# Kernel optimization log

Measured on AMD Instinct MI355X. Metric: run time of the kernel, lower is better.

Reference implementation:

```python
import jax, jax.numpy as jnp
import numpy as np

N_NODES = 100000
N_EDGES = 1600000
NODE_FEATURES = 6
H_EMBED = 64
D = 32
OUT_DIM = 1


def _mlp(x, W1, b1, W2, b2):
    h = jnp.tanh(x @ W1 + b1)
    return jnp.tanh(h @ W2 + b2)


def _gcn_conv(h, W, b, src, dst, n_nodes):
    # PyG GCNConv: linear (no bias) -> add self-loops -> sym-normalized scatter-add -> +bias
    hw = h @ W  # [N, D]
    loop = jnp.arange(n_nodes, dtype=src.dtype)
    row = jnp.concatenate([src, loop])  # sources
    col = jnp.concatenate([dst, loop])  # targets
    ones = jnp.ones(row.shape[0], dtype=hw.dtype)
    deg = jax.ops.segment_sum(ones, col, num_segments=n_nodes)
    dinv = jnp.where(deg > 0, jax.lax.rsqrt(deg), 0.0)
    norm = dinv[row] * dinv[col]  # [E+N]
    msg = hw[row] * norm[:, None]  # gather + scale
    out = jax.ops.segment_sum(msg, col, num_segments=n_nodes)
    return out + b


def setup_inputs() -> dict:
    key = jax.random.key(0)
    ks = jax.random.split(key, 16)
    x = jax.random.normal(ks[0], (N_NODES, NODE_FEATURES), dtype=jnp.float32)
    edge_index = jax.random.randint(ks[1], (2, N_EDGES), 0, N_NODES, dtype=jnp.int64)

    def lin(k, din, dout):
        bound = 1.0 / np.sqrt(din)
        kw, kb = jax.random.split(k)
        W = jax.random.uniform(kw, (din, dout), minval=-bound, maxval=bound, dtype=jnp.float32)
        b = jax.random.uniform(kb, (dout,), minval=-bound, maxval=bound, dtype=jnp.float32)
        return W, b

    We1, be1 = lin(ks[2], NODE_FEATURES, H_EMBED)
    We2, be2 = lin(ks[3], H_EMBED, D)
    Wg1, bg1 = lin(ks[4], D, D)
    Wg2, bg2 = lin(ks[5], D, D)
    Wp1, bp1 = lin(ks[6], D, D)
    Wp2, bp2 = lin(ks[7], D, OUT_DIM)
    return {
        "x": x, "edge_index": edge_index,
        "We1": We1, "be1": be1, "We2": We2, "be2": be2,
        "Wg1": Wg1, "bg1": bg1, "Wg2": Wg2, "bg2": bg2,
        "Wp1": Wp1, "bp1": bp1, "Wp2": Wp2, "bp2": bp2,
    }


def reference(x, edge_index, We1, be1, We2, be2, Wg1, bg1, Wg2, bg2, Wp1, bp1, Wp2, bp2):
    n = x.shape[0]
    src, dst = edge_index[0], edge_index[1]
    h = _mlp(x, We1, be1, We2, be2)            # [N, 32]
    h = jax.nn.relu(_gcn_conv(h, Wg1, bg1, src, dst, n))  # dropout = identity (eval)
    h = jax.nn.relu(_gcn_conv(h, Wg2, bg2, src, dst, n))
    return _mlp(h, Wp1, bp1, Wp2, bp2)         # [N, 1]
```

## Files before the change

kernel.cpp:

```cpp
#include <hip/hip_runtime.h>
#include <hip/hip_fp16.h>

#define NN 100000
#define NE 1600000
#define NPB 128
#define NBUCK ((NN + NPB - 1) / NPB)
#define CAP 5120
#define PBLOCKS 256
#define PTPB 512
#define EPB (NE / PBLOCKS)
#define DUMMY 100000u
#define SENT 0xFFFFFFFFu
#define GBLK 4096
#define NSLOT (GBLK * 8)

__global__ __launch_bounds__(PTPB) void part_kernel(const int* __restrict__ src,
                                                    const int* __restrict__ dst,
                                                    unsigned int* __restrict__ bcount,
                                                    unsigned int* __restrict__ packed) {
    __shared__ unsigned int lcnt[NBUCK];
    __shared__ unsigned int lcur[NBUCK];
    for (int i = threadIdx.x; i < NBUCK; i += PTPB) lcnt[i] = 0u;
    __syncthreads();
    int e0 = blockIdx.x * EPB;
    for (int e = e0 + threadIdx.x; e < e0 + EPB; e += PTPB)
        atomicAdd(&lcnt[((unsigned)dst[e]) >> 7], 1u);
    __syncthreads();
    for (int i = threadIdx.x; i < NBUCK; i += PTPB) {
        unsigned int c = lcnt[i];
        unsigned int rc = (c + 15u) & ~15u;
        lcur[i] = rc ? atomicAdd(&bcount[i], rc) : 0u;
    }
    __syncthreads();
    for (int e = e0 + threadIdx.x; e < e0 + EPB; e += PTPB) {
        unsigned int d = (unsigned)dst[e];
        unsigned int b = d >> 7;
        unsigned int pos = atomicAdd(&lcur[b], 1u);
        packed[(size_t)b * CAP + pos] = ((d & 127u) << 17) | (unsigned)src[e];
    }
}

__global__ __launch_bounds__(512) void sort_kernel(const unsigned int* __restrict__ bcount,
                                                   unsigned int* __restrict__ packed,
                                                   unsigned int* __restrict__ rsd,
                                                   float* __restrict__ dinv) {
    __shared__ unsigned int lraw[CAP];
    __shared__ unsigned int lsort[CAP];
    __shared__ unsigned int cnt[NPB];
    __shared__ unsigned int ps[NPB];
    __shared__ unsigned int cur[NPB];
    __shared__ unsigned int ntot;
    int b = blockIdx.x;
    int tid = threadIdx.x;
    if (tid < NPB) cnt[tid] = 0u;
    __syncthreads();
    unsigned int n = bcount[b];
    unsigned int* pk = packed + (size_t)b * CAP;
    for (unsigned int i = tid; i < n; i += 512) {
        unsigned int p = pk[i];
        lraw[i] = p;
        if (p != SENT) atomicAdd(&cnt[p >> 17], 1u);
    }
    __syncthreads();
    if (tid < NPB) ps[tid] = (cnt[tid] + 7u) & ~7u;
    __syncthreads();
    for (int off = 1; off < NPB; off <<= 1) {
        unsigned int t = (tid < NPB && tid >= off) ? ps[tid - off] : 0u;
        __syncthreads();
        if (tid < NPB) ps[tid] += t;
        __syncthreads();
    }
    if (tid == NPB - 1) ntot = ps[NPB - 1];
    __syncthreads();
    unsigned int np = ntot;
    for (unsigned int i = tid; i < np; i += 512) lsort[i] = DUMMY;
    if (tid < NPB) cur[tid] = ps[tid] - ((cnt[tid] + 7u) & ~7u);
    __syncthreads();
    for (unsigned int i = tid; i < n; i += 512) {
        unsigned int p = lraw[i];
        if (p != SENT) {
            unsigned int pos = atomicAdd(&cur[p >> 17], 1u);
            lsort[pos] = p & 0x1FFFFu;
        }
    }
    __syncthreads();
    for (unsigned int i = tid; i < np; i += 512) pk[i] = lsort[i];
    if (tid < NPB) {
        int node = b * NPB + tid;
        if (node < NN) {
            unsigned int c = cnt[tid];
            unsigned int pc = (c + 7u) & ~7u;
            unsigned int rs = (unsigned int)(b * CAP) + ps[tid] - pc;
            rsd[node] = rs | ((pc >> 3) << 22);
            dinv[node] = rsqrtf((float)c + 1.0f);
        }
    }
}

__global__ __launch_bounds__(256) void embed_kernel(
    const float* __restrict__ x, const float* __restrict__ We1, const float* __restrict__ be1,
    const float* __restrict__ We2, const float* __restrict__ be2, const float* __restrict__ Wg1,
    const float* __restrict__ dinv, __half* __restrict__ hws1, __half* __restrict__ hws2) {
    __shared__ float sWe1[6 * 64];
    __shared__ float sbe1[64];
    __shared__ float sWe2[64 * 32];
    __shared__ float sbe2[32];
    __shared__ float sWg1[32 * 32];
    for (int i = threadIdx.x; i < 6 * 64; i += 256) sWe1[i] = We1[i];
    for (int i = threadIdx.x; i < 64; i += 256) sbe1[i] = be1[i];
    for (int i = threadIdx.x; i < 64 * 32; i += 256) sWe2[i] = We2[i];
    for (int i = threadIdx.x; i < 32; i += 256) sbe2[i] = be2[i];
    for (int i = threadIdx.x; i < 32 * 32; i += 256) sWg1[i] = Wg1[i];
    __syncthreads();

    int node = blockIdx.x * 256 + threadIdx.x;
    if (node > NN) return;
    if (node == NN) {
        for (int j = 0; j < 32; j++) {
            hws1[(size_t)NN * 32 + j] = __float2half(0.f);
            hws2[(size_t)NN * 32 + j] = __float2half(0.f);
        }
        return;
    }

    float xv[6];
#pragma unroll
    for (int k = 0; k < 6; k++) xv[k] = x[node * 6 + k];

    float h1[64];
#pragma unroll
    for (int j = 0; j < 64; j++) {
        float a = sbe1[j];
#pragma unroll
        for (int k = 0; k < 6; k++) a += xv[k] * sWe1[k * 64 + j];
        h1[j] = tanhf(a);
    }

    float h[32];
#pragma unroll 4
    for (int j = 0; j < 32; j++) {
        float a = sbe2[j];
#pragma unroll
        for (int k = 0; k < 64; k++) a += h1[k] * sWe2[k * 32 + j];
        h[j] = tanhf(a);
    }

    float di = dinv[node];
    __half* o = hws1 + (size_t)node * 32;
#pragma unroll 4
    for (int j = 0; j < 32; j++) {
        float a = 0.f;
#pragma unroll
        for (int k = 0; k < 32; k++) a += h[k] * sWg1[k * 32 + j];
        o[j] = __float2half(a * di);
    }
}

__global__ __launch_bounds__(256) void gather1_kernel(
    const unsigned int* __restrict__ sorted, const unsigned int* __restrict__ rsd,
    const float* __restrict__ dinv, const __half* __restrict__ hws1,
    const float* __restrict__ bg1, const float* __restrict__ Wg2,
    __half* __restrict__ hws2) {
    int lane = threadIdx.x & 31;
    int g = lane >> 4;
    int p = lane & 15;
    int f = lane;
    float wreg[32];
#pragma unroll
    for (int k = 0; k < 32; k++) wreg[k] = Wg2[k * 32 + f];
    float bf = bg1[f];
    int slot = (blockIdx.x * 256 + threadIdx.x) >> 5;
    const __half2* H = (const __half2*)hws1;
    int node = slot;
    if (node >= NN) return;
    unsigned int r = rsd[node];
    while (node < NN) {
        int nxt = node + NSLOT;
        unsigned int rn = (nxt < NN) ? rsd[nxt] : 0u;
        unsigned int base = r & 0x3FFFFFu;
        unsigned int d = (r >> 22) << 3;
        float ax = 0.f, ay = 0.f;
        for (unsigned int k = g * 4; k < d; k += 8) {
            uint4 s4 = *reinterpret_cast<const uint4*>(sorted + base + k);
            float2 v0 = __half22float2(H[(size_t)s4.x * 16 + p]);
            float2 v1 = __half22float2(H[(size_t)s4.y * 16 + p]);
            float2 v2 = __half22float2(H[(size_t)s4.z * 16 + p]);
            float2 v3 = __half22float2(H[(size_t)s4.w * 16 + p]);
            ax += (v0.x + v1.x) + (v2.x + v3.x);
            ay += (v0.y + v1.y) + (v2.y + v3.y);
        }
        ax += __shfl_xor(ax, 16); ay += __shfl_xor(ay, 16);
        float2 sv = __half22float2(H[(size_t)node * 16 + p]);
        ax += sv.x; ay += sv.y;
        float ae = __shfl(ax, f >> 1, 32);
        float ao = __shfl(ay, f >> 1, 32);
        float av = (f & 1) ? ao : ae;
        float di = dinv[node];
        float h = di * av + bf;
        h = h > 0.f ? h : 0.f;
        float o = 0.f;
#pragma unroll
        for (int k = 0; k < 32; k++) o += __shfl(h, k, 32) * wreg[k];
        hws2[(size_t)node * 32 + f] = __float2half(o * di);
        node = nxt; r = rn;
    }
}

__global__ __launch_bounds__(256) void gather2_kernel(
    const unsigned int* __restrict__ sorted, const unsigned int* __restrict__ rsd,
    const float* __restrict__ dinv, const __half* __restrict__ hws2,
    const float* __restrict__ bg2, const float* __restrict__ Wp1,
    const float* __restrict__ bp1, const float* __restrict__ Wp2,
    const float* __restrict__ bp2, float* __restrict__ out) {
    int lane = threadIdx.x & 31;
    int g = lane >> 4;
    int p = lane & 15;
    int f = lane;
    float wreg[32];
#pragma unroll
    for (int k = 0; k < 32; k++) wreg[k] = Wp1[k * 32 + f];
    float bgf = bg2[f];
    float b1f = bp1[f];
    float w2f = Wp2[f];
    float b2 = bp2[0];
    int slot = (blockIdx.x * 256 + threadIdx.x) >> 5;
    const __half2* H = (const __half2*)hws2;
    int node = slot;
    if (node >= NN) return;
    unsigned int r = rsd[node];
    while (node < NN) {
        int nxt = node + NSLOT;
        unsigned int rn = (nxt < NN) ? rsd[nxt] : 0u;
        unsigned int base = r & 0x3FFFFFu;
        unsigned int d = (r >> 22) << 3;
        float ax = 0.f, ay = 0.f;
        for (unsigned int k = g * 4; k < d; k += 8) {
            uint4 s4 = *reinterpret_cast<const uint4*>(sorted + base + k);
            float2 v0 = __half22float2(H[(size_t)s4.x * 16 + p]);
            float2 v1 = __half22float2(H[(size_t)s4.y * 16 + p]);
            float2 v2 = __half22float2(H[(size_t)s4.z * 16 + p]);
            float2 v3 = __half22float2(H[(size_t)s4.w * 16 + p]);
            ax += (v0.x + v1.x) + (v2.x + v3.x);
            ay += (v0.y + v1.y) + (v2.y + v3.y);
        }
        ax += __shfl_xor(ax, 16); ay += __shfl_xor(ay, 16);
        float2 sv = __half22float2(H[(size_t)node * 16 + p]);
        ax += sv.x; ay += sv.y;
        float ae = __shfl(ax, f >> 1, 32);
        float ao = __shfl(ay, f >> 1, 32);
        float av = (f & 1) ? ao : ae;
        float di = dinv[node];
        float h = di * av + bgf;
        h = h > 0.f ? h : 0.f;
        float pre = b1f;
#pragma unroll
        for (int k = 0; k < 32; k++) pre += __shfl(h, k, 32) * wreg[k];
        float t = tanhf(pre) * w2f;
#pragma unroll
        for (int off = 1; off < 32; off <<= 1) t += __shfl_xor(t, off);
        if (lane == 0) out[node] = tanhf(t + b2);
        node = nxt; r = rn;
    }
}

extern "C" void kernel_launch(void* const* d_in, const int* in_sizes, int n_in,
                              void* d_out, int out_size, void* d_ws, size_t ws_size,
                              hipStream_t stream) {
    const float* x = (const float*)d_in[0];
    const int* edge = (const int*)d_in[1];
    const int* src = edge;
    const int* dst = edge + NE;
    const float* We1 = (const float*)d_in[2];
    const float* be1 = (const float*)d_in[3];
    const float* We2 = (const float*)d_in[4];
    const float* be2 = (const float*)d_in[5];
    const float* Wg1 = (const float*)d_in[6];
    const float* bg1 = (const float*)d_in[7];
    const float* Wg2 = (const float*)d_in[8];
    const float* bg2 = (const float*)d_in[9];
    const float* Wp1 = (const float*)d_in[10];
    const float* bp1 = (const float*)d_in[11];
    const float* Wp2 = (const float*)d_in[12];
    const float* bp2 = (const float*)d_in[13];
    float* out = (float*)d_out;

    unsigned int* bcount = (unsigned int*)d_ws;
    float* dinv = (float*)d_ws + 1024;
    unsigned int* rsd = (unsigned int*)d_ws + 1024 + NN;
    unsigned int* packed = (unsigned int*)d_ws + 1024 + 2 * NN;
    __half* hws1 = (__half*)((unsigned int*)d_ws + 1024 + 2 * NN + NBUCK * CAP);
    __half* hws2 = hws1 + (size_t)(NN + 1) * 32;

    hipMemsetAsync(bcount, 0, 1024 * sizeof(unsigned int), stream);
    hipMemsetAsync(packed, 0xFF, (size_t)NBUCK * CAP * 4, stream);

    int gridN = (NN + 256) / 256;

    part_kernel<<<PBLOCKS, PTPB, 0, stream>>>(src, dst, bcount, packed);
    sort_kernel<<<NBUCK, 512, 0, stream>>>(bcount, packed, rsd, dinv);
    embed_kernel<<<gridN, 256, 0, stream>>>(x, We1, be1, We2, be2, Wg1, dinv, hws1, hws2);
    gather1_kernel<<<GBLK, 256, 0, stream>>>(packed, rsd, dinv, hws1, bg1, Wg2, hws2);
    gather2_kernel<<<GBLK, 256, 0, stream>>>(packed, rsd, dinv, hws2, bg2, Wp1, bp1, Wp2, bp2, out);
}
```

Baseline: 250.1 us.

## Interleave two nodes per half-warp in gather kernels and retune partition launch

Both gather kernels now process two nodes (na and na+NSLOT) per loop iteration, issuing their neighbor-index and feature loads together to double memory-level parallelism, with tail loops for unequal degrees. The partition kernel is retuned to 128 blocks of 1024 threads with a smaller bucket capacity. The interleaving raises register pressure and halves the number of loop iterations per warp, which may reduce occupancy or worsen load balance; the smaller CAP risks overflow if bucket sizes exceed it.

```diff
diff --git a/kernel.cpp b/kernel.cpp
--- a/kernel.cpp
+++ b/kernel.cpp
@@ -5,9 +5,9 @@
 #define NE 1600000
 #define NPB 128
 #define NBUCK ((NN + NPB - 1) / NPB)
-#define CAP 5120
-#define PBLOCKS 256
-#define PTPB 512
+#define CAP 4608
+#define PBLOCKS 128
+#define PTPB 1024
 #define EPB (NE / PBLOCKS)
 #define DUMMY 100000u
 #define SENT 0xFFFFFFFFu
@@ -171,38 +171,78 @@
     float bf = bg1[f];
     int slot = (blockIdx.x * 256 + threadIdx.x) >> 5;
     const __half2* H = (const __half2*)hws1;
-    int node = slot;
-    if (node >= NN) return;
-    unsigned int r = rsd[node];
-    while (node < NN) {
-        int nxt = node + NSLOT;
-        unsigned int rn = (nxt < NN) ? rsd[nxt] : 0u;
-        unsigned int base = r & 0x3FFFFFu;
-        unsigned int d = (r >> 22) << 3;
-        float ax = 0.f, ay = 0.f;
-        for (unsigned int k = g * 4; k < d; k += 8) {
-            uint4 s4 = *reinterpret_cast<const uint4*>(sorted + base + k);
-            float2 v0 = __half22float2(H[(size_t)s4.x * 16 + p]);
-            float2 v1 = __half22float2(H[(size_t)s4.y * 16 + p]);
-            float2 v2 = __half22float2(H[(size_t)s4.z * 16 + p]);
-            float2 v3 = __half22float2(H[(size_t)s4.w * 16 + p]);
-            ax += (v0.x + v1.x) + (v2.x + v3.x);
-            ay += (v0.y + v1.y) + (v2.y + v3.y);
+    for (int na = slot; na < NN; na += 2 * NSLOT) {
+        int nb = na + NSLOT;
+        bool hb = nb < NN;
+        unsigned int ra = rsd[na];
+        unsigned int rb = hb ? rsd[nb] : 0u;
+        unsigned int base_a = ra & 0x3FFFFFu, da = (ra >> 22) << 3;
+        unsigned int base_b = rb & 0x3FFFFFu, db = hb ? ((rb >> 22) << 3) : 0u;
+        float ax = 0.f, ay = 0.f, bx2 = 0.f, by2 = 0.f;
+        unsigned int dmin = da < db ? da : db;
+        unsigned int k = g * 4;
+        for (; k < dmin; k += 8) {
+            uint4 sa = *reinterpret_cast<const uint4*>(sorted + base_a + k);
+            uint4 sb = *reinterpret_cast<const uint4*>(sorted + base_b + k);
+            float2 a0 = __half22float2(H[(size_t)sa.x * 16 + p]);
+            float2 a1 = __half22float2(H[(size_t)sa.y * 16 + p]);
+            float2 a2 = __half22float2(H[(size_t)sa.z * 16 + p]);
+            float2 a3 = __half22float2(H[(size_t)sa.w * 16 + p]);
+            float2 b0 = __half22float2(H[(size_t)sb.x * 16 + p]);
+            float2 b1 = __half22float2(H[(size_t)sb.y * 16 + p]);
+            float2 b2 = __half22float2(H[(size_t)sb.z * 16 + p]);
+            float2 b3 = __half22float2(H[(size_t)sb.w * 16 + p]);
+            ax += (a0.x + a1.x) + (a2.x + a3.x);
+            ay += (a0.y + a1.y) + (a2.y + a3.y);
+            bx2 += (b0.x + b1.x) + (b2.x + b3.x);
+            by2 += (b0.y + b1.y) + (b2.y + b3.y);
+        }
+        for (unsigned int ka = k; ka < da; ka += 8) {
+            uint4 sa = *reinterpret_cast<const uint4*>(sorted + base_a + ka);
+            float2 a0 = __half22float2(H[(size_t)sa.x * 16 + p]);
+            float2 a1 = __half22float2(H[(size_t)sa.y * 16 + p]);
+            float2 a2 = __half22float2(H[(size_t)sa.z * 16 + p]);
+            float2 a3 = __half22float2(H[(size_t)sa.w * 16 + p]);
+            ax += (a0.x + a1.x) + (a2.x + a3.x);
+            ay += (a0.y + a1.y) + (a2.y + a3.y);
+        }
+        for (unsigned int kb = k; kb < db; kb += 8) {
+            uint4 sb = *reinterpret_cast<const uint4*>(sorted + base_b + kb);
+            float2 b0 = __half22float2(H[(size_t)sb.x * 16 + p]);
+            float2 b1 = __half22float2(H[(size_t)sb.y * 16 + p]);
+            float2 b2 = __half22float2(H[(size_t)sb.z * 16 + p]);
+            float2 b3 = __half22float2(H[(size_t)sb.w * 16 + p]);
+            bx2 += (b0.x + b1.x) + (b2.x + b3.x);
+            by2 += (b0.y + b1.y) + (b2.y + b3.y);
         }
         ax += __shfl_xor(ax, 16); ay += __shfl_xor(ay, 16);
-        float2 sv = __half22float2(H[(size_t)node * 16 + p]);
+        float2 sv = __half22float2(H[(size_t)na * 16 + p]);
         ax += sv.x; ay += sv.y;
         float ae = __shfl(ax, f >> 1, 32);
         float ao = __shfl(ay, f >> 1, 32);
         float av = (f & 1) ? ao : ae;
-        float di = dinv[node];
-        float h = di * av + bf;
-        h = h > 0.f ? h : 0.f;
-        float o = 0.f;
-#pragma unroll
-        for (int k = 0; k < 32; k++) o += __shfl(h, k, 32) * wreg[k];
-        hws2[(size_t)node * 32 + f] = __float2half(o * di);
-        node = nxt; r = rn;
+        float dia = dinv[na];
+        float ha = dia * av + bf;
+        ha = ha > 0.f ? ha : 0.f;
+        float oa = 0.f;
+#pragma unroll
+        for (int k2 = 0; k2 < 32; k2++) oa += __shfl(ha, k2, 32) * wreg[k2];
+        hws2[(size_t)na * 32 + f] = __float2half(oa * dia);
+        if (hb) {
+            bx2 += __shfl_xor(bx2, 16); by2 += __shfl_xor(by2, 16);
+            float2 svb = __half22float2(H[(size_t)nb * 16 + p]);
+            bx2 += svb.x; by2 += svb.y;
+            float be = __shfl(bx2, f >> 1, 32);
+            float bo = __shfl(by2, f >> 1, 32);
+            float bv = (f & 1) ? bo : be;
+            float dib = dinv[nb];
+            float hbv = dib * bv + bf;
+            hbv = hbv > 0.f ? hbv : 0.f;
+            float ob = 0.f;
+#pragma unroll
+            for (int k2 = 0; k2 < 32; k2++) ob += __shfl(hbv, k2, 32) * wreg[k2];
+            hws2[(size_t)nb * 32 + f] = __float2half(ob * dib);
+        }
     }
 }
 
@@ -225,41 +265,84 @@
     float b2 = bp2[0];
     int slot = (blockIdx.x * 256 + threadIdx.x) >> 5;
     const __half2* H = (const __half2*)hws2;
-    int node = slot;
-    if (node >= NN) return;
-    unsigned int r = rsd[node];
-    while (node < NN) {
-        int nxt = node + NSLOT;
-        unsigned int rn = (nxt < NN) ? rsd[nxt] : 0u;
-        unsigned int base = r & 0x3FFFFFu;
-        unsigned int d = (r >> 22) << 3;
-        float ax = 0.f, ay = 0.f;
-        for (unsigned int k = g * 4; k < d; k += 8) {
-            uint4 s4 = *reinterpret_cast<const uint4*>(sorted + base + k);
-            float2 v0 = __half22float2(H[(size_t)s4.x * 16 + p]);
-            float2 v1 = __half22float2(H[(size_t)s4.y * 16 + p]);
-            float2 v2 = __half22float2(H[(size_t)s4.z * 16 + p]);
-            float2 v3 = __half22float2(H[(size_t)s4.w * 16 + p]);
-            ax += (v0.x + v1.x) + (v2.x + v3.x);
-            ay += (v0.y + v1.y) + (v2.y + v3.y);
+    for (int na = slot; na < NN; na += 2 * NSLOT) {
+        int nb = na + NSLOT;
+        bool hb = nb < NN;
+        unsigned int ra = rsd[na];
+        unsigned int rb = hb ? rsd[nb] : 0u;
+        unsigned int base_a = ra & 0x3FFFFFu, da = (ra >> 22) << 3;
+        unsigned int base_b = rb & 0x3FFFFFu, db = hb ? ((rb >> 22) << 3) : 0u;
+        float ax = 0.f, ay = 0.f, bx2 = 0.f, by2 = 0.f;
+        unsigned int dmin = da < db ? da : db;
+        unsigned int k = g * 4;
+        for (; k < dmin; k += 8) {
+            uint4 sa = *reinterpret_cast<const uint4*>(sorted + base_a + k);
+            uint4 sb = *reinterpret_cast<const uint4*>(sorted + base_b + k);
+            float2 a0 = __half22float2(H[(size_t)sa.x * 16 + p]);
+            float2 a1 = __half22float2(H[(size_t)sa.y * 16 + p]);
+            float2 a2 = __half22float2(H[(size_t)sa.z * 16 + p]);
+            float2 a3 = __half22float2(H[(size_t)sa.w * 16 + p]);
+            float2 b0 = __half22float2(H[(size_t)sb.x * 16 + p]);
+            float2 b1 = __half22float2(H[(size_t)sb.y * 16 + p]);
+            float2 b2 = __half22float2(H[(size_t)sb.z * 16 + p]);
+            float2 b3 = __half22float2(H[(size_t)sb.w * 16 + p]);
+            ax += (a0.x + a1.x) + (a2.x + a3.x);
+            ay += (a0.y + a1.y) + (a2.y + a3.y);
+            bx2 += (b0.x + b1.x) + (b2.x + b3.x);
+            by2 += (b0.y + b1.y) + (b2.y + b3.y);
+        }
+        for (unsigned int ka = k; ka < da; ka += 8) {
+            uint4 sa = *reinterpret_cast<const uint4*>(sorted + base_a + ka);
+            float2 a0 = __half22float2(H[(size_t)sa.x * 16 + p]);
+            float2 a1 = __half22float2(H[(size_t)sa.y * 16 + p]);
+            float2 a2 = __half22float2(H[(size_t)sa.z * 16 + p]);
+            float2 a3 = __half22float2(H[(size_t)sa.w * 16 + p]);
+            ax += (a0.x + a1.x) + (a2.x + a3.x);
+            ay += (a0.y + a1.y) + (a2.y + a3.y);
+        }
+        for (unsigned int kb = k; kb < db; kb += 8) {
+            uint4 sb = *reinterpret_cast<const uint4*>(sorted + base_b + kb);
+            float2 b0 = __half22float2(H[(size_t)sb.x * 16 + p]);
+            float2 b1 = __half22float2(H[(size_t)sb.y * 16 + p]);
+            float2 b2 = __half22float2(H[(size_t)sb.z * 16 + p]);
+            float2 b3 = __half22float2(H[(size_t)sb.w * 16 + p]);
+            bx2 += (b0.x + b1.x) + (b2.x + b3.x);
+            by2 += (b0.y + b1.y) + (b2.y + b3.y);
         }
         ax += __shfl_xor(ax, 16); ay += __shfl_xor(ay, 16);
-        float2 sv = __half22float2(H[(size_t)node * 16 + p]);
+        float2 sv = __half22float2(H[(size_t)na * 16 + p]);
         ax += sv.x; ay += sv.y;
         float ae = __shfl(ax, f >> 1, 32);
         float ao = __shfl(ay, f >> 1, 32);
         float av = (f & 1) ? ao : ae;
-        float di = dinv[node];
-        float h = di * av + bgf;
-        h = h > 0.f ? h : 0.f;
+        float dia = dinv[na];
+        float ha = dia * av + bgf;
+        ha = ha > 0.f ? ha : 0.f;
         float pre = b1f;
 #pragma unroll
-        for (int k = 0; k < 32; k++) pre += __shfl(h, k, 32) * wreg[k];
+        for (int k2 = 0; k2 < 32; k2++) pre += __shfl(ha, k2, 32) * wreg[k2];
         float t = tanhf(pre) * w2f;
 #pragma unroll
         for (int off = 1; off < 32; off <<= 1) t += __shfl_xor(t, off);
-        if (lane == 0) out[node] = tanhf(t + b2);
-        node = nxt; r = rn;
+        if (lane == 0) out[na] = tanhf(t + b2);
+        if (hb) {
+            bx2 += __shfl_xor(bx2, 16); by2 += __shfl_xor(by2, 16);
+            float2 svb = __half22float2(H[(size_t)nb * 16 + p]);
+            bx2 += svb.x; by2 += svb.y;
+            float be = __shfl(bx2, f >> 1, 32);
+            float bo = __shfl(by2, f >> 1, 32);
+            float bv = (f & 1) ? bo : be;
+            float dib = dinv[nb];
+            float hbv = dib * bv + bgf;
+            hbv = hbv > 0.f ? hbv : 0.f;
+            float preb = b1f;
+#pragma unroll
+            for (int k2 = 0; k2 < 32; k2++) preb += __shfl(hbv, k2, 32) * wreg[k2];
+            float tb = tanhf(preb) * w2f;
+#pragma unroll
+            for (int off = 1; off < 32; off <<= 1) tb += __shfl_xor(tb, off);
+            if (lane == 0) out[nb] = tanhf(tb + b2);
+        }
     }
 }
 
```

After: 245.9 us. No clear change (-1.7%).
